# Kernel optimization log

Measured on AMD Instinct MI355X. Metric: run time of the kernel, lower is better.

Reference implementation:

```python
import jax, jax.numpy as jnp
import numpy as np

VOCAB_SIZE = 119547  # bert-base-multilingual-cased
B, S, H = 64, 512, 768


def setup_inputs() -> dict:
    key = jax.random.key(0)
    k1, k2, k3, k4 = jax.random.split(key, 4)
    hidden_states = jax.random.normal(k1, (B, S, H), dtype=jnp.float32)
    input_ids = jax.random.randint(k2, (B, S), 0, VOCAB_SIZE, dtype=jnp.int64)
    attention_mask = jnp.ones((B, S), dtype=jnp.int32)
    W1 = jax.random.normal(k3, (H, H), dtype=jnp.float32) * (1.0 / np.sqrt(H))
    b1 = jnp.zeros((H,), dtype=jnp.float32)
    W2 = jax.random.normal(k4, (H, 1), dtype=jnp.float32) * (1.0 / np.sqrt(H))
    b2 = jnp.zeros((1,), dtype=jnp.float32)
    return {"hidden_states": hidden_states, "input_ids": input_ids,
            "attention_mask": attention_mask, "W1": W1, "b1": b1, "W2": W2, "b2": b2}


def reference(hidden_states, input_ids, attention_mask, W1, b1, W2, b2):
    # token_importance MLP (dropout = identity at eval): [B,S,H] -> [B,S]
    h = jax.nn.relu(jnp.einsum('bsh,hk->bsk', hidden_states, W1) + b1)
    importance = (jnp.einsum('bsh,ho->bso', h, W2) + b2)[..., 0]  # [B,S]
    token_weights = jnp.log1p(jax.nn.relu(importance)) * attention_mask.astype(jnp.float32)
    # scatter-max into vocab-sized sparse doc vector.
    # Masked positions have weight 0; buffer init 0 and weights >= 0, so
    # scattering 0 is equivalent to skipping them (matches the torch loop).
    batch_idx = jnp.arange(hidden_states.shape[0])[:, None]  # [B,1]
    sparse_repr = jnp.zeros((hidden_states.shape[0], VOCAB_SIZE), dtype=token_weights.dtype)
    sparse_repr = sparse_repr.at[batch_idx, input_ids].max(token_weights)
    return sparse_repr, token_weights
```

## Files before the change

kernel.cpp:

```cpp
#include <hip/hip_runtime.h>
#include <math.h>
#include <stdint.h>

#define VOCAB 119547
#define NB    64
#define NS    512
#define NH    768
#define M_TOT (NB * NS)

typedef _Float16 half8_t __attribute__((ext_vector_type(8)));
typedef _Float16 half4_t __attribute__((ext_vector_type(4)));
typedef float f32x4 __attribute__((ext_vector_type(4)));

#define WAITVM(N) asm volatile("s_waitcnt vmcnt(" #N ")" ::: "memory")
#define WAITLGKM() asm volatile("s_waitcnt lgkmcnt(0)" ::: "memory")
#define SCHEDB() __builtin_amdgcn_sched_barrier(0)

__device__ __forceinline__ void gload_lds16(const void* g, void* l) {
    __builtin_amdgcn_global_load_lds(
        (const __attribute__((address_space(1))) uint32_t*)g,
        (__attribute__((address_space(3))) uint32_t*)l, 16, 0, 0);
}

__global__ void prep_all(const float* __restrict__ X, const float* __restrict__ W1,
                         float4* __restrict__ sparse4, float4* __restrict__ imp4,
                         _Float16* __restrict__ Xh, _Float16* __restrict__ W1T) {
    long i = (long)blockIdx.x * blockDim.x + threadIdx.x;
    long stride = (long)gridDim.x * blockDim.x;
    const float4 z = make_float4(0.f, 0.f, 0.f, 0.f);
    const long nsp4 = (long)NB * VOCAB / 4;
    for (long j = i; j < nsp4; j += stride) sparse4[j] = z;
    for (long j = i; j < M_TOT / 4; j += stride) imp4[j] = z;
    const long nx8 = (long)M_TOT * NH / 8;
    const float4* X4 = (const float4*)X;
    half8_t* Xh8 = (half8_t*)Xh;
    for (long j = i; j < nx8; j += stride) {
        float4 a = X4[2 * j], b = X4[2 * j + 1];
        half8_t h;
        h[0] = (_Float16)a.x; h[1] = (_Float16)a.y;
        h[2] = (_Float16)a.z; h[3] = (_Float16)a.w;
        h[4] = (_Float16)b.x; h[5] = (_Float16)b.y;
        h[6] = (_Float16)b.z; h[7] = (_Float16)b.w;
        Xh8[j] = h;
    }
    const long nw8 = (long)NH * NH / 8;
    half8_t* W1T8 = (half8_t*)W1T;
    for (long j = i; j < nw8; j += stride) {
        int n  = (int)(j / (NH / 8));
        int k8 = (int)(j % (NH / 8)) * 8;
        half8_t h;
#pragma unroll
        for (int q = 0; q < 8; ++q) h[q] = (_Float16)W1[(long)(k8 + q) * NH + n];
        W1T8[j] = h;
    }
}

__global__ __launch_bounds__(256, 3) void gemm_f16(
    const _Float16* __restrict__ Xh,
    const _Float16* __restrict__ W1T,
    const float* __restrict__ b1,
    const float* __restrict__ W2v,
    float* __restrict__ imp)
{
    __shared__ __align__(16) _Float16 As[3][128 * 32];
    __shared__ __align__(16) _Float16 Bs[3][128 * 32];

    const int tid  = threadIdx.x;
    const int lane = tid & 63;
    const int wid  = tid >> 6;
    const int wm   = wid >> 1;
    const int wn   = wid & 1;

    const int bid = blockIdx.x;
    const int wg  = (bid & 7) * 192 + (bid >> 3);
    const int nt  = wg % 6;
    const int mt  = wg / 6;
    const int m0  = mt * 128;
    const int n0  = nt * 128;

    const int c0 = tid, c1 = tid + 256;
    const int r0 = c0 >> 2, r1 = c1 >> 2;
    const int sk0 = ((c0 & 3) ^ ((r0 >> 1) & 3)) * 8;
    const int sk1 = ((c1 & 3) ^ ((r1 >> 1) & 3)) * 8;
    const _Float16* gA0 = Xh  + (long)(m0 + r0) * NH + sk0;
    const _Float16* gA1 = Xh  + (long)(m0 + r1) * NH + sk1;
    const _Float16* gB0 = W1T + (long)(n0 + r0) * NH + sk0;
    const _Float16* gB1 = W1T + (long)(n0 + r1) * NH + sk1;

    const int lr = lane & 15;
    const int ls = lane >> 4;
    const int s2 = ls ^ ((lr >> 1) & 3);
    int offA[4], offB[4];
#pragma unroll
    for (int f = 0; f < 4; ++f) {
        offA[f] = (wm * 64 + f * 16 + lr) * 32 + s2 * 8;
        offB[f] = (wn * 64 + f * 16 + lr) * 32 + s2 * 8;
    }

    f32x4 acc[4][4];
#pragma unroll
    for (int a = 0; a < 4; ++a)
#pragma unroll
        for (int b = 0; b < 4; ++b) acc[a][b] = (f32x4){0.f, 0.f, 0.f, 0.f};

#define STAGE(T, BUF)                                                       \
    gload_lds16(gA0 + (T) * 32, As[BUF] + c0 * 8);                          \
    gload_lds16(gA1 + (T) * 32, As[BUF] + c1 * 8);                          \
    gload_lds16(gB0 + (T) * 32, Bs[BUF] + c0 * 8);                          \
    gload_lds16(gB1 + (T) * 32, Bs[BUF] + c1 * 8);

#define COMPUTE(BUF)                                                        \
    {                                                                       \
        half8_t af[4], bf[4];                                               \
        _Pragma("unroll") for (int f = 0; f < 4; ++f)                       \
            af[f] = *(const half8_t*)(As[BUF] + offA[f]);                   \
        _Pragma("unroll") for (int f = 0; f < 4; ++f)                       \
            bf[f] = *(const half8_t*)(Bs[BUF] + offB[f]);                   \
        _Pragma("unroll") for (int a = 0; a < 4; ++a)                       \
            _Pragma("unroll") for (int b = 0; b < 4; ++b)                   \
                acc[a][b] = __builtin_amdgcn_mfma_f32_16x16x32_f16(         \
                    af[a], bf[b], acc[a][b], 0, 0, 0);                      \
    }

#define KSTEP(TSTG, CURB, STGB)                                             \
    STAGE(TSTG, STGB);                                                      \
    SCHEDB();                                                               \
    COMPUTE(CURB);                                                          \
    WAITVM(4);                                                              \
    WAITLGKM();                                                             \
    __builtin_amdgcn_s_barrier();                                           \
    SCHEDB();

    STAGE(0, 0);
    STAGE(1, 1);
    WAITVM(4);
    WAITLGKM();
    __builtin_amdgcn_s_barrier();
    SCHEDB();

#pragma unroll 1
    for (int tt = 0; tt < 7; ++tt) {
        const int t3 = 3 * tt;
        KSTEP(t3 + 2, 0, 2);
        KSTEP(t3 + 3, 1, 0);
        KSTEP(t3 + 4, 2, 1);
    }
    KSTEP(23, 0, 2);
    COMPUTE(1);
    WAITVM(0);
    WAITLGKM();
    __builtin_amdgcn_s_barrier();
    SCHEDB();
    COMPUTE(2);

#undef STAGE
#undef COMPUTE
#undef KSTEP

    float b1v[4], w2v[4];
#pragma unroll
    for (int f = 0; f < 4; ++f) {
        int col = n0 + wn * 64 + f * 16 + lr;
        b1v[f] = b1[col];
        w2v[f] = W2v[col];
    }
#pragma unroll
    for (int a = 0; a < 4; ++a)
#pragma unroll
        for (int reg = 0; reg < 4; ++reg) {
            float p = 0.f;
#pragma unroll
            for (int f = 0; f < 4; ++f) {
                float h = fmaxf(acc[a][f][reg] + b1v[f], 0.f);
                p = fmaf(h, w2v[f], p);
            }
            p += __shfl_xor(p, 1);
            p += __shfl_xor(p, 2);
            p += __shfl_xor(p, 4);
            p += __shfl_xor(p, 8);
            if (lr == 0) {
                int row = m0 + wm * 64 + a * 16 + ls * 4 + reg;
                atomicAdd(&imp[row], p);
            }
        }
}

__global__ void finalize(const float* __restrict__ imp,
                         const float* __restrict__ b2,
                         const int* __restrict__ mask,
                         const int* __restrict__ ids,
                         float* __restrict__ tw_out,
                         float* __restrict__ sparse) {
    int i = blockIdx.x * blockDim.x + threadIdx.x;
    if (i >= M_TOT) return;
    float v = fmaxf(imp[i] + b2[0], 0.f);
    float tw = log1pf(v) * (float)mask[i];
    tw_out[i] = tw;
    int b  = i >> 9;
    int id = ids[i];
    unsigned int* addr = (unsigned int*)&sparse[(long)b * VOCAB + id];
    atomicMax(addr, __float_as_uint(tw));
}

__global__ __launch_bounds__(256) void gemm_importance(
    const float* __restrict__ X, const float* __restrict__ W1,
    const float* __restrict__ b1, const float* __restrict__ W2v,
    float* __restrict__ imp)
{
    __shared__ float As_[16][64];
    __shared__ float Bs_[16][128];
    const int tid = threadIdx.x;
    const int m0 = blockIdx.x * 64, n0 = blockIdx.y * 128;
    const int tx = tid & 31, ty = tid >> 5;
    float acc[8][4];
#pragma unroll
    for (int r = 0; r < 8; ++r)
#pragma unroll
        for (int c = 0; c < 4; ++c) acc[r][c] = 0.f;
    const int arow = tid >> 2, ac = (tid & 3) * 4;
    const float* Xp = X + (long)(m0 + arow) * NH + ac;
    for (int k0 = 0; k0 < NH; k0 += 16) {
        float4 av = *(const float4*)(Xp + k0);
        As_[ac + 0][arow] = av.x; As_[ac + 1][arow] = av.y;
        As_[ac + 2][arow] = av.z; As_[ac + 3][arow] = av.w;
        int f = tid, br = f >> 5, bc = (f & 31) * 4;
        *(float4*)&Bs_[br][bc] = *(const float4*)&W1[(long)(k0 + br) * NH + n0 + bc];
        f = tid + 256; br = f >> 5; bc = (f & 31) * 4;
        *(float4*)&Bs_[br][bc] = *(const float4*)&W1[(long)(k0 + br) * NH + n0 + bc];
        __syncthreads();
#pragma unroll
        for (int k = 0; k < 16; ++k) {
            float4 a0 = *(const float4*)&As_[k][ty * 8];
            float4 a1 = *(const float4*)&As_[k][ty * 8 + 4];
            float4 bv = *(const float4*)&Bs_[k][tx * 4];
            float a[8] = {a0.x, a0.y, a0.z, a0.w, a1.x, a1.y, a1.z, a1.w};
            float bb[4] = {bv.x, bv.y, bv.z, bv.w};
#pragma unroll
            for (int r = 0; r < 8; ++r)
#pragma unroll
                for (int c = 0; c < 4; ++c)
                    acc[r][c] = fmaf(a[r], bb[c], acc[r][c]);
        }
        __syncthreads();
    }
    float b1v[4], w2v[4];
#pragma unroll
    for (int c = 0; c < 4; ++c) {
        int col = n0 + tx * 4 + c;
        b1v[c] = b1[col]; w2v[c] = W2v[col];
    }
#pragma unroll
    for (int r = 0; r < 8; ++r) {
        float p = 0.f;
#pragma unroll
        for (int c = 0; c < 4; ++c)
            p = fmaf(fmaxf(acc[r][c] + b1v[c], 0.f), w2v[c], p);
#pragma unroll
        for (int mdel = 16; mdel >= 1; mdel >>= 1) p += __shfl_xor(p, mdel);
        if (tx == 0) atomicAdd(&imp[m0 + ty * 8 + r], p);
    }
}

extern "C" void kernel_launch(void* const* d_in, const int* in_sizes, int n_in,
                              void* d_out, int out_size, void* d_ws, size_t ws_size,
                              hipStream_t stream) {
    const float* X    = (const float*)d_in[0];
    const int*   ids  = (const int*)d_in[1];
    const int*   mask = (const int*)d_in[2];
    const float* W1   = (const float*)d_in[3];
    const float* b1   = (const float*)d_in[4];
    const float* W2   = (const float*)d_in[5];
    const float* b2   = (const float*)d_in[6];

    float* sparse = (float*)d_out;
    float* tw_out = sparse + (long)NB * VOCAB;
    float* imp    = (float*)d_ws;

    const size_t impB = (size_t)M_TOT * 4;
    const size_t XhB  = (size_t)M_TOT * NH * 2;
    const size_t W1TB = (size_t)NH * NH * 2;

    if (ws_size >= impB + XhB + W1TB) {
        _Float16* Xh  = (_Float16*)((char*)d_ws + impB);
        _Float16* W1T = (_Float16*)((char*)d_ws + impB + XhB);
        prep_all<<<4096, 256, 0, stream>>>(X, W1, (float4*)sparse, (float4*)imp,
                                           Xh, W1T);
        gemm_f16<<<(M_TOT / 128) * (NH / 128), 256, 0, stream>>>(
            Xh, W1T, b1, W2, imp);
    } else {
        hipMemsetAsync(sparse, 0, (size_t)NB * VOCAB * 4, stream);
        hipMemsetAsync(imp, 0, impB, stream);
        dim3 grid(M_TOT / 64, NH / 128);
        gemm_importance<<<grid, 256, 0, stream>>>(X, W1, b1, W2, imp);
    }
    finalize<<<M_TOT / 256, 256, 0, stream>>>(imp, b2, mask, ids, tw_out, sparse);
}
```

Measured before the change: 236.2 us.

## Fuse fp32-to-fp16 conversion of activations into GEMM LDS staging

Removes the separate pass that converts the hidden states to fp16 in a workspace buffer. The GEMM now streams fp32 activations straight into LDS with a swizzled layout and converts them to fp16 when building MFMA fragments. This cuts one full read and write of the large activation tensor. In exchange each N-tile re-reads fp32 A, doubling A traffic per tile, and the larger LDS footprint lowers occupancy to 2 blocks.

```diff
diff --git a/kernel.cpp b/kernel.cpp
--- a/kernel.cpp
+++ b/kernel.cpp
@@ -22,27 +22,15 @@
         (__attribute__((address_space(3))) uint32_t*)l, 16, 0, 0);
 }
 
-__global__ void prep_all(const float* __restrict__ X, const float* __restrict__ W1,
-                         float4* __restrict__ sparse4, float4* __restrict__ imp4,
-                         _Float16* __restrict__ Xh, _Float16* __restrict__ W1T) {
+__global__ void prep_small(const float* __restrict__ W1,
+                           float4* __restrict__ sparse4, float4* __restrict__ imp4,
+                           _Float16* __restrict__ W1T) {
     long i = (long)blockIdx.x * blockDim.x + threadIdx.x;
     long stride = (long)gridDim.x * blockDim.x;
     const float4 z = make_float4(0.f, 0.f, 0.f, 0.f);
     const long nsp4 = (long)NB * VOCAB / 4;
     for (long j = i; j < nsp4; j += stride) sparse4[j] = z;
     for (long j = i; j < M_TOT / 4; j += stride) imp4[j] = z;
-    const long nx8 = (long)M_TOT * NH / 8;
-    const float4* X4 = (const float4*)X;
-    half8_t* Xh8 = (half8_t*)Xh;
-    for (long j = i; j < nx8; j += stride) {
-        float4 a = X4[2 * j], b = X4[2 * j + 1];
-        half8_t h;
-        h[0] = (_Float16)a.x; h[1] = (_Float16)a.y;
-        h[2] = (_Float16)a.z; h[3] = (_Float16)a.w;
-        h[4] = (_Float16)b.x; h[5] = (_Float16)b.y;
-        h[6] = (_Float16)b.z; h[7] = (_Float16)b.w;
-        Xh8[j] = h;
-    }
     const long nw8 = (long)NH * NH / 8;
     half8_t* W1T8 = (half8_t*)W1T;
     for (long j = i; j < nw8; j += stride) {
@@ -55,14 +43,14 @@
     }
 }
 
-__global__ __launch_bounds__(256, 3) void gemm_f16(
-    const _Float16* __restrict__ Xh,
+__global__ __launch_bounds__(256, 2) void gemm_f16(
+    const float* __restrict__ X,
     const _Float16* __restrict__ W1T,
     const float* __restrict__ b1,
     const float* __restrict__ W2v,
     float* __restrict__ imp)
 {
-    __shared__ __align__(16) _Float16 As[3][128 * 32];
+    __shared__ __align__(16) float    As32[3][128 * 32];
     __shared__ __align__(16) _Float16 Bs[3][128 * 32];
 
     const int tid  = threadIdx.x;
@@ -78,24 +66,32 @@
     const int m0  = mt * 128;
     const int n0  = nt * 128;
 
+    const float* gA[4];
+#pragma unroll
+    for (int q = 0; q < 4; ++q) {
+        int c = tid + 256 * q;
+        int rowA = c >> 3, w = c & 7;
+        gA[q] = X + (long)(m0 + rowA) * NH + ((w ^ (rowA & 7)) * 4);
+    }
+
     const int c0 = tid, c1 = tid + 256;
     const int r0 = c0 >> 2, r1 = c1 >> 2;
     const int sk0 = ((c0 & 3) ^ ((r0 >> 1) & 3)) * 8;
     const int sk1 = ((c1 & 3) ^ ((r1 >> 1) & 3)) * 8;
-    const _Float16* gA0 = Xh  + (long)(m0 + r0) * NH + sk0;
-    const _Float16* gA1 = Xh  + (long)(m0 + r1) * NH + sk1;
     const _Float16* gB0 = W1T + (long)(n0 + r0) * NH + sk0;
     const _Float16* gB1 = W1T + (long)(n0 + r1) * NH + sk1;
 
     const int lr = lane & 15;
     const int ls = lane >> 4;
+    int offA0[4];
+#pragma unroll
+    for (int f = 0; f < 4; ++f)
+        offA0[f] = (wm * 64 + f * 16 + lr) * 32 + (((2 * ls) ^ (lr & 7)) * 4);
     const int s2 = ls ^ ((lr >> 1) & 3);
-    int offA[4], offB[4];
-#pragma unroll
-    for (int f = 0; f < 4; ++f) {
-        offA[f] = (wm * 64 + f * 16 + lr) * 32 + s2 * 8;
+    int offB[4];
+#pragma unroll
+    for (int f = 0; f < 4; ++f)
         offB[f] = (wn * 64 + f * 16 + lr) * 32 + s2 * 8;
-    }
 
     f32x4 acc[4][4];
 #pragma unroll
@@ -104,16 +100,26 @@
         for (int b = 0; b < 4; ++b) acc[a][b] = (f32x4){0.f, 0.f, 0.f, 0.f};
 
 #define STAGE(T, BUF)                                                       \
-    gload_lds16(gA0 + (T) * 32, As[BUF] + c0 * 8);                          \
-    gload_lds16(gA1 + (T) * 32, As[BUF] + c1 * 8);                          \
+    gload_lds16(gA[0] + (T) * 32, As32[BUF] + (tid +   0) * 4);             \
+    gload_lds16(gA[1] + (T) * 32, As32[BUF] + (tid + 256) * 4);             \
+    gload_lds16(gA[2] + (T) * 32, As32[BUF] + (tid + 512) * 4);             \
+    gload_lds16(gA[3] + (T) * 32, As32[BUF] + (tid + 768) * 4);             \
     gload_lds16(gB0 + (T) * 32, Bs[BUF] + c0 * 8);                          \
     gload_lds16(gB1 + (T) * 32, Bs[BUF] + c1 * 8);
 
 #define COMPUTE(BUF)                                                        \
     {                                                                       \
         half8_t af[4], bf[4];                                               \
-        _Pragma("unroll") for (int f = 0; f < 4; ++f)                       \
-            af[f] = *(const half8_t*)(As[BUF] + offA[f]);                   \
+        _Pragma("unroll") for (int f = 0; f < 4; ++f) {                     \
+            float4 klo = *(const float4*)(&As32[BUF][offA0[f]]);            \
+            float4 khi = *(const float4*)(&As32[BUF][offA0[f] ^ 4]);        \
+            half8_t a_;                                                     \
+            a_[0] = (_Float16)klo.x; a_[1] = (_Float16)klo.y;               \
+            a_[2] = (_Float16)klo.z; a_[3] = (_Float16)klo.w;               \
+            a_[4] = (_Float16)khi.x; a_[5] = (_Float16)khi.y;               \
+            a_[6] = (_Float16)khi.z; a_[7] = (_Float16)khi.w;               \
+            af[f] = a_;                                                     \
+        }                                                                   \
         _Pragma("unroll") for (int f = 0; f < 4; ++f)                       \
             bf[f] = *(const half8_t*)(Bs[BUF] + offB[f]);                   \
         _Pragma("unroll") for (int a = 0; a < 4; ++a)                       \
@@ -126,14 +132,14 @@
     STAGE(TSTG, STGB);                                                      \
     SCHEDB();                                                               \
     COMPUTE(CURB);                                                          \
-    WAITVM(4);                                                              \
+    WAITVM(6);                                                              \
     WAITLGKM();                                                             \
     __builtin_amdgcn_s_barrier();                                           \
     SCHEDB();
 
     STAGE(0, 0);
     STAGE(1, 1);
-    WAITVM(4);
+    WAITVM(6);
     WAITLGKM();
     __builtin_amdgcn_s_barrier();
     SCHEDB();
@@ -277,16 +283,13 @@
     float* imp    = (float*)d_ws;
 
     const size_t impB = (size_t)M_TOT * 4;
-    const size_t XhB  = (size_t)M_TOT * NH * 2;
     const size_t W1TB = (size_t)NH * NH * 2;
 
-    if (ws_size >= impB + XhB + W1TB) {
-        _Float16* Xh  = (_Float16*)((char*)d_ws + impB);
-        _Float16* W1T = (_Float16*)((char*)d_ws + impB + XhB);
-        prep_all<<<4096, 256, 0, stream>>>(X, W1, (float4*)sparse, (float4*)imp,
-                                           Xh, W1T);
+    if (ws_size >= impB + W1TB) {
+        _Float16* W1T = (_Float16*)((char*)d_ws + impB);
+        prep_small<<<2048, 256, 0, stream>>>(W1, (float4*)sparse, (float4*)imp, W1T);
         gemm_f16<<<(M_TOT / 128) * (NH / 128), 256, 0, stream>>>(
-            Xh, W1T, b1, W2, imp);
+            X, W1T, b1, W2, imp);
     } else {
         hipMemsetAsync(sparse, 0, (size_t)NB * VOCAB * 4, stream);
         hipMemsetAsync(imp, 0, impB, stream);
```

Measured after the change: 247.7 us. 1.05x slower.
